# Kernel tuning notes

Measured on AMD Instinct MI355X. Metric: run time of the kernel, lower is better.

Reference implementation:

```python
import jax, jax.numpy as jnp
import numpy as np

NUM_NETS = 2_000_000
PINS_PER_NET = 4
NUM_PINS = NUM_NETS * PINS_PER_NET


def setup_inputs() -> dict:
    key = jax.random.key(0)
    k1, k2, k3 = jax.random.split(key, 3)
    num_slrX, num_slrY = 1, 4
    # pin positions already expressed in SLR-grid units: x in [0, num_slrX), y in [0, num_slrY)
    pos = jax.random.uniform(k1, (NUM_PINS, 2), jnp.float32) * jnp.array(
        [float(max(num_slrX, 1)), float(max(num_slrY, 1))], jnp.float32)
    # CSR netpin structure: each net owns PINS_PER_NET pins, flat list is a permutation of all pins
    flat_netpin = jax.random.permutation(k2, NUM_PINS).astype(jnp.int32)
    netpin_start = (jnp.arange(NUM_NETS + 1, dtype=jnp.int32) * PINS_PER_NET)
    net_ids = jnp.repeat(jnp.arange(NUM_NETS, dtype=jnp.int32), PINS_PER_NET)
    net_weights = jax.random.uniform(k3, (NUM_NETS,), jnp.float32, minval=0.5, maxval=1.5)
    net_mask = jnp.ones((NUM_NETS,), jnp.bool_)
    pin_mask = jnp.zeros((NUM_PINS,), jnp.bool_)
    inv_gamma = jnp.float32(2.0)  # 1 / gamma, gamma = 0.5
    return dict(pos=pos, flat_netpin=flat_netpin, netpin_start=netpin_start,
                net_ids=net_ids, net_weights=net_weights, net_mask=net_mask,
                pin_mask=pin_mask, inv_gamma=inv_gamma,
                num_slrX=num_slrX, num_slrY=num_slrY)


def reference(pos, flat_netpin, netpin_start, net_ids, net_weights, net_mask,
              pin_mask, inv_gamma, num_slrX, num_slrY):
    """Weighted-average SLL: per-net log-sum-exp weighted-average span of pin
    SLR coordinates, per dimension, counted only for dims with >1 SLR."""
    n = net_weights.shape[0]
    p = pos[flat_netpin]  # [P, 2] gather pin coords in CSR order
    # numerically-stable exp weights per net (segment max/min shift)
    mx = jax.ops.segment_max(p, net_ids, num_segments=n)  # [N, 2]
    mn = jax.ops.segment_min(p, net_ids, num_segments=n)  # [N, 2]
    ep = jnp.exp((p - mx[net_ids]) * inv_gamma)   # exp(+x/gamma), shifted
    en = jnp.exp((mn[net_ids] - p) * inv_gamma)   # exp(-x/gamma), shifted
    s_ep = jax.ops.segment_sum(ep, net_ids, num_segments=n)
    s_xep = jax.ops.segment_sum(p * ep, net_ids, num_segments=n)
    s_en = jax.ops.segment_sum(en, net_ids, num_segments=n)
    s_xen = jax.ops.segment_sum(p * en, net_ids, num_segments=n)
    wa = s_xep / s_ep - s_xen / s_en  # [N, 2] weighted-average span per dim
    dim_on = jnp.array([num_slrX > 1, num_slrY > 1], dtype=wa.dtype)  # only multi-SLR dims
    per_net = jnp.sum(wa * dim_on, axis=1)  # [N]
    return jnp.sum(jnp.where(net_mask, net_weights * per_net, jnp.float32(0.0)))
```

## Files before the change

kernel.cpp:

```cpp
#include <hip/hip_runtime.h>


__device__ __forceinline__ float wa4(float a, float b, float c, float d, float ig) {
    float mx = fmaxf(fmaxf(a, b), fmaxf(c, d));
    float mn = fminf(fminf(a, b), fminf(c, d));
    float ea = __expf((a - mx) * ig);
    float eb = __expf((b - mx) * ig);
    float ec = __expf((c - mx) * ig);
    float ed = __expf((d - mx) * ig);
    float na = __expf((mn - a) * ig);
    float nb = __expf((mn - b) * ig);
    float nc = __expf((mn - c) * ig);
    float nd = __expf((mn - d) * ig);
    float s_ep  = ea + eb + ec + ed;
    float s_xep = a * ea + b * eb + c * ec + d * ed;
    float s_en  = na + nb + nc + nd;
    float s_xen = a * na + b * nb + c * nc + d * nd;
    return s_xep / s_ep - s_xen / s_en;
}

__global__ void zero_out_kernel(float* __restrict__ out) {
    out[0] = 0.0f;
}

__global__ __launch_bounds__(256) void wasll_kernel(
    const float2* __restrict__ pos,
    const int4*   __restrict__ fnp4,
    const float*  __restrict__ net_weights,
    const float*  __restrict__ inv_gamma_p,
    const int*    __restrict__ slrx_p,
    const int*    __restrict__ slry_p,
    float*        __restrict__ out,
    int num_nets)
{
    const float ig   = inv_gamma_p[0];
    const float dimx = (slrx_p[0] > 1) ? 1.0f : 0.0f;
    const float dimy = (slry_p[0] > 1) ? 1.0f : 0.0f;

    int net = blockIdx.x * blockDim.x + threadIdx.x;
    float val = 0.0f;
    if (net < num_nets) {
        int4 idx = fnp4[net];
        float2 p0 = pos[idx.x];
        float2 p1 = pos[idx.y];
        float2 p2 = pos[idx.z];
        float2 p3 = pos[idx.w];
        float wa_x = wa4(p0.x, p1.x, p2.x, p3.x, ig);
        float wa_y = wa4(p0.y, p1.y, p2.y, p3.y, ig);
        val = net_weights[net] * (dimx * wa_x + dimy * wa_y);
    }

    #pragma unroll
    for (int off = 32; off > 0; off >>= 1)
        val += __shfl_down(val, off, 64);

    __shared__ float smem[4];
    int lane = threadIdx.x & 63;
    int wid  = threadIdx.x >> 6;
    if (lane == 0) smem[wid] = val;
    __syncthreads();
    if (threadIdx.x == 0) {
        float s = smem[0] + smem[1] + smem[2] + smem[3];
        atomicAdd(out, s);
    }
}

extern "C" void kernel_launch(void* const* d_in, const int* in_sizes, int n_in,
                              void* d_out, int out_size, void* d_ws, size_t ws_size,
                              hipStream_t stream) {
    const float2* pos         = (const float2*)d_in[0];
    const int4*   fnp4        = (const int4*)d_in[1];
    const float*  net_weights = (const float*)d_in[4];
    const float*  inv_gamma   = (const float*)d_in[7];
    const int*    slrx        = (const int*)d_in[8];
    const int*    slry        = (const int*)d_in[9];
    float*        out         = (float*)d_out;
    const int num_nets        = in_sizes[4];

    hipLaunchKernelGGL(zero_out_kernel, dim3(1), dim3(1), 0, stream, out);

    const int block = 256;
    const int grid  = (num_nets + block - 1) / block;
    hipLaunchKernelGGL(wasll_kernel, dim3(grid), dim3(block), 0, stream,
                       pos, fnp4, net_weights, inv_gamma, slrx, slry,
                       out, num_nets);
}
```

Before: 293.8 us.

## Replace random pin gather with two-pass bucket partition for locality

```diff
diff --git a/kernel.cpp b/kernel.cpp
--- a/kernel.cpp
+++ b/kernel.cpp
@@ -1,17 +1,21 @@
 #include <hip/hip_runtime.h>
-
+#include <stdint.h>
+
+
+#define PINB_SHIFT 15
+#define PINB_SIZE  (1 << PINB_SHIFT)
+#define JB_SHIFT   14
+#define JB_SIZE    (1 << JB_SHIFT)
+#define P1_CHUNK   4096
+#define P2_CHUNK   4096
+#define MAX_PINB   256
+#define MAX_JB     512
 
 __device__ __forceinline__ float wa4(float a, float b, float c, float d, float ig) {
-    float mx = fmaxf(fmaxf(a, b), fmaxf(c, d));
-    float mn = fminf(fminf(a, b), fminf(c, d));
-    float ea = __expf((a - mx) * ig);
-    float eb = __expf((b - mx) * ig);
-    float ec = __expf((c - mx) * ig);
-    float ed = __expf((d - mx) * ig);
-    float na = __expf((mn - a) * ig);
-    float nb = __expf((mn - b) * ig);
-    float nc = __expf((mn - c) * ig);
-    float nd = __expf((mn - d) * ig);
+    float ea = __expf(a * ig), eb = __expf(b * ig);
+    float ec = __expf(c * ig), ed = __expf(d * ig);
+    float na = __expf(-a * ig), nb = __expf(-b * ig);
+    float nc = __expf(-c * ig), nd = __expf(-d * ig);
     float s_ep  = ea + eb + ec + ed;
     float s_xep = a * ea + b * eb + c * ec + d * ed;
     float s_en  = na + nb + nc + nd;
@@ -19,69 +23,307 @@
     return s_xep / s_ep - s_xen / s_en;
 }
 
-__global__ void zero_out_kernel(float* __restrict__ out) {
-    out[0] = 0.0f;
-}
-
-__global__ __launch_bounds__(256) void wasll_kernel(
-    const float2* __restrict__ pos,
-    const int4*   __restrict__ fnp4,
-    const float*  __restrict__ net_weights,
-    const float*  __restrict__ inv_gamma_p,
-    const int*    __restrict__ slrx_p,
-    const int*    __restrict__ slry_p,
-    float*        __restrict__ out,
-    int num_nets)
+__global__ void zero_out_kernel(float* __restrict__ out) { out[0] = 0.0f; }
+
+__global__ void init_cursors_kernel(unsigned* __restrict__ cur1, int n_pinb,
+                                    unsigned* __restrict__ cur2, int n_jb) {
+    int t = threadIdx.x;
+    for (int i = t; i < n_pinb; i += blockDim.x) cur1[i] = (unsigned)i * PINB_SIZE;
+    for (int i = t; i < n_jb;   i += blockDim.x) cur2[i] = (unsigned)i * JB_SIZE;
+}
+
+__global__ __launch_bounds__(256) void p1_partition(
+    const int* __restrict__ fnp, int NP, int n_pinb,
+    uint2* __restrict__ ent1, unsigned* __restrict__ cur1)
 {
-    const float ig   = inv_gamma_p[0];
-    const float dimx = (slrx_p[0] > 1) ? 1.0f : 0.0f;
-    const float dimy = (slry_p[0] > 1) ? 1.0f : 0.0f;
-
+    __shared__ uint2 staged[P1_CHUNK];
+    __shared__ unsigned hist[MAX_PINB], scn[MAX_PINB];
+    __shared__ unsigned lcnt[MAX_PINB], gbase[MAX_PINB];
+    const int base  = blockIdx.x * P1_CHUNK;
+    const int valid = min(P1_CHUNK, NP - base);
+    const int t = threadIdx.x;
+
+    if (t < n_pinb) { hist[t] = 0; lcnt[t] = 0; }
+    __syncthreads();
+
+    unsigned pins[16];
+    #pragma unroll
+    for (int m = 0; m < 16; ++m) {
+        int k = t + 256 * m;
+        pins[m] = 0u;
+        if (k < valid) {
+            pins[m] = (unsigned)fnp[base + k];
+            atomicAdd(&hist[pins[m] >> PINB_SHIFT], 1u);
+        }
+    }
+    __syncthreads();
+
+    if (t < n_pinb) scn[t] = hist[t];
+    __syncthreads();
+    #pragma unroll
+    for (int off = 1; off < MAX_PINB; off <<= 1) {
+        unsigned v = 0;
+        if (t < n_pinb && t >= off) v = scn[t - off];
+        __syncthreads();
+        if (t < n_pinb) scn[t] += v;
+        __syncthreads();
+    }
+    if (t < n_pinb) {
+        unsigned ex = scn[t] - hist[t];
+        scn[t] = ex;
+        gbase[t] = atomicAdd(&cur1[t], hist[t]);
+    }
+    __syncthreads();
+
+    #pragma unroll
+    for (int m = 0; m < 16; ++m) {
+        int k = t + 256 * m;
+        if (k < valid) {
+            unsigned pin = pins[m];
+            unsigned b = pin >> PINB_SHIFT;
+            unsigned pos = scn[b] + atomicAdd(&lcnt[b], 1u);
+            staged[pos] = make_uint2(pin, (unsigned)(base + k));
+        }
+    }
+    __syncthreads();
+
+    for (int k = t; k < valid; k += 256) {
+        uint2 e = staged[k];
+        unsigned b = e.x >> PINB_SHIFT;
+        unsigned dst = gbase[b] + ((unsigned)k - scn[b]);
+        ent1[dst] = e;
+    }
+}
+
+__global__ __launch_bounds__(512) void p2_gather(
+    const uint2* __restrict__ ent1, const float* __restrict__ posf,
+    const int* __restrict__ slrx_p,
+    int NP, int n_pinb, int n_jb,
+    uint2* __restrict__ ent2, float* __restrict__ xout,
+    unsigned* __restrict__ cur2)
+{
+    const int x   = blockIdx.x & 7;
+    const int g   = blockIdx.x >> 3;
+    const int r   = g >> 3;
+    const int sub = g & 7;
+    const int b   = x + 8 * r;
+    if (b >= n_pinb) return;
+    const int count_b = min(PINB_SIZE, NP - b * PINB_SIZE);
+    const int sbase   = sub * P2_CHUNK;
+    const int valid   = min(P2_CHUNK, count_b - sbase);
+    if (valid <= 0) return;
+
+    const bool dimx = (slrx_p[0] > 1);
+    __shared__ uint2 staged[P2_CHUNK];
+    __shared__ float xstag[P2_CHUNK];
+    __shared__ unsigned hist[MAX_JB], scn[MAX_JB];
+    __shared__ unsigned lcnt[MAX_JB], gbase[MAX_JB];
+    const int t = threadIdx.x;
+
+    if (t < n_jb) { hist[t] = 0; lcnt[t] = 0; }
+    __syncthreads();
+
+    uint2 e[8]; float yv[8], xv[8];
+    const int ebase = b * PINB_SIZE + sbase;
+    #pragma unroll
+    for (int m = 0; m < 8; ++m) {
+        int k = t + 512 * m;
+        e[m] = (k < valid) ? ent1[ebase + k] : make_uint2(0u, 0u);
+    }
+    #pragma unroll
+    for (int m = 0; m < 8; ++m) {
+        int k = t + 512 * m;
+        yv[m] = 0.f; xv[m] = 0.f;
+        if (k < valid) {
+            yv[m] = posf[2u * e[m].x + 1u];
+            if (dimx) xv[m] = posf[2u * e[m].x];
+        }
+    }
+    #pragma unroll
+    for (int m = 0; m < 8; ++m) {
+        int k = t + 512 * m;
+        if (k < valid) atomicAdd(&hist[e[m].y >> JB_SHIFT], 1u);
+    }
+    __syncthreads();
+
+    if (t < n_jb) scn[t] = hist[t];
+    __syncthreads();
+    #pragma unroll
+    for (int off = 1; off < MAX_JB; off <<= 1) {
+        unsigned v = 0;
+        if (t < n_jb && t >= off) v = scn[t - off];
+        __syncthreads();
+        if (t < n_jb) scn[t] += v;
+        __syncthreads();
+    }
+    if (t < n_jb) {
+        unsigned ex = scn[t] - hist[t];
+        scn[t] = ex;
+        gbase[t] = atomicAdd(&cur2[t], hist[t]);
+    }
+    __syncthreads();
+
+    #pragma unroll
+    for (int m = 0; m < 8; ++m) {
+        int k = t + 512 * m;
+        if (k < valid) {
+            unsigned jb = e[m].y >> JB_SHIFT;
+            unsigned pos = scn[jb] + atomicAdd(&lcnt[jb], 1u);
+            staged[pos] = make_uint2(e[m].y, __float_as_uint(yv[m]));
+            if (dimx) xstag[pos] = xv[m];
+        }
+    }
+    __syncthreads();
+
+    for (int k = t; k < valid; k += 512) {
+        uint2 s = staged[k];
+        unsigned jb = s.x >> JB_SHIFT;
+        unsigned dst = gbase[jb] + ((unsigned)k - scn[jb]);
+        ent2[dst] = s;
+        if (dimx) xout[dst] = xstag[k];
+    }
+}
+
+__global__ __launch_bounds__(256) void p3_compute(
+    const uint2* __restrict__ ent2, const float* __restrict__ xin,
+    const float* __restrict__ wts, const float* __restrict__ ig_p,
+    const int* __restrict__ slrx_p, const int* __restrict__ slry_p,
+    int NP, float* __restrict__ out)
+{
+    __shared__ float ytmp[JB_SIZE];
+    const int jb = blockIdx.x;
+    const int base_j = jb * JB_SIZE;
+    const int nslots = min(JB_SIZE, NP - base_j);
+    const int t = threadIdx.x;
+    const float ig = ig_p[0];
+    const bool dimx = (slrx_p[0] > 1), dimy = (slry_p[0] > 1);
+    float val = 0.f;
+
+    if (!dimx) {
+        for (int k = t; k < nslots; k += 256) {
+            uint2 e = ent2[base_j + k];
+            ytmp[e.x - (unsigned)base_j] = __uint_as_float(e.y);
+        }
+        __syncthreads();
+        const int nnets = nslots >> 2, bnet = base_j >> 2;
+        for (int i = t; i < nnets; i += 256) {
+            float wy = wa4(ytmp[4*i], ytmp[4*i+1], ytmp[4*i+2], ytmp[4*i+3], ig);
+            val += wts[bnet + i] * (dimy ? wy : 0.f);
+        }
+    } else {
+        for (int h = 0; h < 2; ++h) {
+            const int h0 = base_j + h * (JB_SIZE / 2);
+            const int hn = min(JB_SIZE / 2, NP - h0);
+            if (hn <= 0) break;
+            __syncthreads();
+            for (int k = t; k < nslots; k += 256) {
+                uint2 e = ent2[base_j + k];
+                int rel = (int)e.x - h0;
+                if (rel >= 0 && rel < hn) {
+                    ytmp[rel] = __uint_as_float(e.y);
+                    ytmp[(JB_SIZE / 2) + rel] = xin[base_j + k];
+                }
+            }
+            __syncthreads();
+            const int nnets = hn >> 2, bnet = h0 >> 2;
+            for (int i = t; i < nnets; i += 256) {
+                float wy = wa4(ytmp[4*i], ytmp[4*i+1], ytmp[4*i+2], ytmp[4*i+3], ig);
+                float wx = wa4(ytmp[(JB_SIZE/2)+4*i], ytmp[(JB_SIZE/2)+4*i+1],
+                               ytmp[(JB_SIZE/2)+4*i+2], ytmp[(JB_SIZE/2)+4*i+3], ig);
+                val += wts[bnet + i] * ((dimx ? wx : 0.f) + (dimy ? wy : 0.f));
+            }
+        }
+    }
+
+    #pragma unroll
+    for (int off = 32; off > 0; off >>= 1) val += __shfl_down(val, off, 64);
+    __syncthreads();
+    if ((t & 63) == 0) ytmp[t >> 6] = val;
+    __syncthreads();
+    if (t == 0) atomicAdd(out, ytmp[0] + ytmp[1] + ytmp[2] + ytmp[3]);
+}
+
+__global__ __launch_bounds__(256) void wasll_fallback(
+    const float2* __restrict__ pos, const int4* __restrict__ fnp4,
+    const float* __restrict__ net_weights, const float* __restrict__ inv_gamma_p,
+    const int* __restrict__ slrx_p, const int* __restrict__ slry_p,
+    float* __restrict__ out, int num_nets)
+{
+    const float ig = inv_gamma_p[0];
+    const float dx = (slrx_p[0] > 1) ? 1.0f : 0.0f;
+    const float dy = (slry_p[0] > 1) ? 1.0f : 0.0f;
     int net = blockIdx.x * blockDim.x + threadIdx.x;
     float val = 0.0f;
     if (net < num_nets) {
         int4 idx = fnp4[net];
-        float2 p0 = pos[idx.x];
-        float2 p1 = pos[idx.y];
-        float2 p2 = pos[idx.z];
-        float2 p3 = pos[idx.w];
-        float wa_x = wa4(p0.x, p1.x, p2.x, p3.x, ig);
-        float wa_y = wa4(p0.y, p1.y, p2.y, p3.y, ig);
-        val = net_weights[net] * (dimx * wa_x + dimy * wa_y);
-    }
-
-    #pragma unroll
-    for (int off = 32; off > 0; off >>= 1)
-        val += __shfl_down(val, off, 64);
-
+        float2 p0 = pos[idx.x], p1 = pos[idx.y], p2 = pos[idx.z], p3 = pos[idx.w];
+        val = net_weights[net] * (dx * wa4(p0.x, p1.x, p2.x, p3.x, ig)
+                                + dy * wa4(p0.y, p1.y, p2.y, p3.y, ig));
+    }
+    #pragma unroll
+    for (int off = 32; off > 0; off >>= 1) val += __shfl_down(val, off, 64);
     __shared__ float smem[4];
-    int lane = threadIdx.x & 63;
-    int wid  = threadIdx.x >> 6;
-    if (lane == 0) smem[wid] = val;
-    __syncthreads();
-    if (threadIdx.x == 0) {
-        float s = smem[0] + smem[1] + smem[2] + smem[3];
-        atomicAdd(out, s);
-    }
+    if ((threadIdx.x & 63) == 0) smem[threadIdx.x >> 6] = val;
+    __syncthreads();
+    if (threadIdx.x == 0)
+        atomicAdd(out, smem[0] + smem[1] + smem[2] + smem[3]);
 }
 
 extern "C" void kernel_launch(void* const* d_in, const int* in_sizes, int n_in,
                               void* d_out, int out_size, void* d_ws, size_t ws_size,
                               hipStream_t stream) {
-    const float2* pos         = (const float2*)d_in[0];
-    const int4*   fnp4        = (const int4*)d_in[1];
-    const float*  net_weights = (const float*)d_in[4];
-    const float*  inv_gamma   = (const float*)d_in[7];
-    const int*    slrx        = (const int*)d_in[8];
-    const int*    slry        = (const int*)d_in[9];
-    float*        out         = (float*)d_out;
-    const int num_nets        = in_sizes[4];
+    const float* posf        = (const float*)d_in[0];
+    const int*   fnp         = (const int*)d_in[1];
+    const float* net_weights = (const float*)d_in[4];
+    const float* inv_gamma   = (const float*)d_in[7];
+    const int*   slrx        = (const int*)d_in[8];
+    const int*   slry        = (const int*)d_in[9];
+    float*       out         = (float*)d_out;
+    const int    N  = in_sizes[4];
+    const int    NP = in_sizes[1];
 
     hipLaunchKernelGGL(zero_out_kernel, dim3(1), dim3(1), 0, stream, out);
 
-    const int block = 256;
-    const int grid  = (num_nets + block - 1) / block;
-    hipLaunchKernelGGL(wasll_kernel, dim3(grid), dim3(block), 0, stream,
-                       pos, fnp4, net_weights, inv_gamma, slrx, slry,
-                       out, num_nets);
-}
+    const int n_pinb = (NP + PINB_SIZE - 1) >> PINB_SHIFT;
+    const int n_jb   = (NP + JB_SIZE - 1) >> JB_SHIFT;
+
+    size_t off = 0;
+    auto carve = [&](size_t bytes) { size_t o = off; off += (bytes + 255) & ~size_t(255); return o; };
+    size_t o_ent1 = carve((size_t)n_pinb * PINB_SIZE * sizeof(uint2));
+    size_t o_ent2 = carve((size_t)n_jb * JB_SIZE * sizeof(uint2));
+    size_t o_xout = carve((size_t)n_jb * JB_SIZE * sizeof(float));
+    size_t o_cur1 = carve((size_t)n_pinb * sizeof(unsigned));
+    size_t o_cur2 = carve((size_t)n_jb * sizeof(unsigned));
+
+    const bool ok = (NP == 4 * N) && (n_pinb <= MAX_PINB) && (n_jb <= MAX_JB) &&
+                    (off <= ws_size);
+    if (!ok) {
+        const int block = 256, grid = (N + block - 1) / block;
+        hipLaunchKernelGGL(wasll_fallback, dim3(grid), dim3(block), 0, stream,
+                           (const float2*)posf, (const int4*)fnp, net_weights,
+                           inv_gamma, slrx, slry, out, N);
+        return;
+    }
+
+    char* ws = (char*)d_ws;
+    uint2*    ent1 = (uint2*)(ws + o_ent1);
+    uint2*    ent2 = (uint2*)(ws + o_ent2);
+    float*    xout = (float*)(ws + o_xout);
+    unsigned* cur1 = (unsigned*)(ws + o_cur1);
+    unsigned* cur2 = (unsigned*)(ws + o_cur2);
+
+    hipLaunchKernelGGL(init_cursors_kernel, dim3(1), dim3(512), 0, stream,
+                       cur1, n_pinb, cur2, n_jb);
+
+    const int g1 = (NP + P1_CHUNK - 1) / P1_CHUNK;
+    hipLaunchKernelGGL(p1_partition, dim3(g1), dim3(256), 0, stream,
+                       fnp, NP, n_pinb, ent1, cur1);
+
+    const int rounds = (n_pinb + 7) / 8;
+    const int g2 = 8 * 8 * rounds;
+    hipLaunchKernelGGL(p2_gather, dim3(g2), dim3(512), 0, stream,
+                       ent1, posf, slrx, NP, n_pinb, n_jb, ent2, xout, cur2);
+
+    hipLaunchKernelGGL(p3_compute, dim3(n_jb), dim3(256), 0, stream,
+                       ent2, xout, net_weights, inv_gamma, slrx, slry, NP, out);
+}
```

Measured after the change: 318.8 us. 1.08x slower.
